# Performance work log

Measured on AMD Instinct MI355X. Metric: run time of the kernel, lower is better.

The kernel has to match this reference:

```python
import jax, jax.numpy as jnp
import numpy as np

B = 4
P0, P1, P2 = 196608, 49152, 12288
DEG = 8
K = 4
EPS = 1e-5


def _cheb_conv(x, cols, vals, W, b):
    """Chebyshev graph conv. x: (B,P,Cin); cols/vals: (P,DEG) fixed-degree sparse L;
    W: (K*Cin, Cout); b: (Cout,). Recursion: T0=x, T1=Lx, Tk=2 L T_{k-1} - T_{k-2}."""
    def lmul(y):  # sparse matvec per batch/channel: (B,P,C) -> (B,P,C)
        return jnp.einsum('pd,bpdc->bpc', vals, y[:, cols, :])
    t0 = x
    t1 = lmul(t0)
    terms = [t0, t1]
    for _ in range(K - 2):
        t2 = 2.0 * lmul(t1) - t0
        terms.append(t2)
        t0, t1 = t1, t2
    xk = jnp.concatenate(terms, axis=-1)  # (B,P,K*Cin)
    return xk @ W + b


def _layernorm(h, g, bt):
    mu = jnp.mean(h, axis=-1, keepdims=True)
    var = jnp.mean(jnp.square(h - mu), axis=-1, keepdims=True)
    return g * (h - mu) / jnp.sqrt(var + EPS) + bt


def _avg_pool4(h):  # HEALPix nested-order average pooling: (B,P,C) -> (B,P//4,C)
    Bh, P, C = h.shape
    return h.reshape(Bh, P // 4, 4, C).mean(axis=2)


def setup_inputs() -> dict:
    key = jax.random.key(0)
    ks = jax.random.split(key, 16)
    cin, c1, c2, c3 = 16, 64, 128, 256
    hid, emb = 512, 256

    def glorot(k, shape):
        fan_in = shape[0]
        return jax.random.normal(k, shape, jnp.float32) / np.sqrt(fan_in)

    inp = {
        'x': jax.random.normal(ks[0], (B, P0, cin), jnp.float32),
        'cols1': jax.random.randint(ks[1], (P0, DEG), 0, P0),
        'vals1': 0.2 * jax.random.normal(ks[2], (P0, DEG), jnp.float32),
        'cols2': jax.random.randint(ks[3], (P1, DEG), 0, P1),
        'vals2': 0.2 * jax.random.normal(ks[4], (P1, DEG), jnp.float32),
        'cols3': jax.random.randint(ks[5], (P2, DEG), 0, P2),
        'vals3': 0.2 * jax.random.normal(ks[6], (P2, DEG), jnp.float32),
        'W1': glorot(ks[7], (K * cin, c1)), 'b1': jnp.zeros((c1,), jnp.float32),
        'g1': jnp.ones((c1,), jnp.float32), 'bt1': jnp.zeros((c1,), jnp.float32),
        'W2': glorot(ks[8], (K * c1, c2)), 'b2': jnp.zeros((c2,), jnp.float32),
        'g2': jnp.ones((c2,), jnp.float32), 'bt2': jnp.zeros((c2,), jnp.float32),
        'W3': glorot(ks[9], (K * c2, c3)), 'b3': jnp.zeros((c3,), jnp.float32),
        'g3': jnp.ones((c3,), jnp.float32), 'bt3': jnp.zeros((c3,), jnp.float32),
        'mW1': glorot(ks[10], (c3, hid)), 'mb1': jnp.zeros((hid,), jnp.float32),
        'mW2': glorot(ks[11], (hid, emb)), 'mb2': jnp.zeros((emb,), jnp.float32),
    }
    return inp


def reference(x, cols1, vals1, cols2, vals2, cols3, vals3,
              W1, b1, g1, bt1, W2, b2, g2, bt2, W3, b3, g3, bt3,
              mW1, mb1, mW2, mb2):
    # Stage 1: ChebConv -> LayerNorm -> ReLU -> avg pool (4:1)
    h = _cheb_conv(x, cols1, vals1, W1, b1)
    h = jax.nn.relu(_layernorm(h, g1, bt1))
    h = _avg_pool4(h)
    # Stage 2
    h = _cheb_conv(h, cols2, vals2, W2, b2)
    h = jax.nn.relu(_layernorm(h, g2, bt2))
    h = _avg_pool4(h)
    # Stage 3 (last stage: no pooling)
    h = _cheb_conv(h, cols3, vals3, W3, b3)
    h = jax.nn.relu(_layernorm(h, g3, bt3))
    # Global mean pool over pixels, then MLP head (Linear-ReLU-Linear)
    z = h.mean(axis=1)                     # (B, 256)
    z = jax.nn.relu(z @ mW1 + mb1)
    z = z @ mW2 + mb2                      # (B, 256)
    return z
```

## Files before the change

### kernel.cpp

```cpp
#include <hip/hip_runtime.h>
#include <hip/hip_bf16.h>

namespace {

constexpr int B  = 4;
constexpr int P0 = 196608, P1 = 49152, P2 = 12288;
constexpr int DEG = 8;
constexpr float EPS = 1e-5f;
constexpr int NBLK3 = (P2 * B) / 64;
constexpr int RSL = 16;
constexpr int RPB = NBLK3 / RSL;

typedef __attribute__((ext_vector_type(4))) float f32x4;
typedef __attribute__((ext_vector_type(8))) short s16x8;

__device__ __forceinline__ float b2f(unsigned short u) {
    union { unsigned int i; float f; } c; c.i = (unsigned int)u << 16; return c.f;
}
__device__ __forceinline__ unsigned short f2b(float f) {
    __hip_bfloat16 h = __float2bfloat16(f);
    return *reinterpret_cast<unsigned short*>(&h);
}

__global__ __launch_bounds__(256)
void x2p_kernel(const float* __restrict__ in, unsigned short* __restrict__ out)
{
    long idx = (long)blockIdx.x * blockDim.x + threadIdx.x;
    if (idx >= (long)P0 * B * 2) return;
    int  h = (int)(idx & 1);
    int  b = (int)((idx >> 1) & 3);
    long p = idx >> 3;
    const float* src = in + ((size_t)b * P0 + p) * 16 + h * 8;
    float4 v0 = *(const float4*)src;
    float4 v1 = *(const float4*)(src + 4);
    union { uint4 u; unsigned short s[8]; } o;
    o.s[0] = f2b(v0.x); o.s[1] = f2b(v0.y); o.s[2] = f2b(v0.z); o.s[3] = f2b(v0.w);
    o.s[4] = f2b(v1.x); o.s[5] = f2b(v1.y); o.s[6] = f2b(v1.z); o.s[7] = f2b(v1.w);
    *(uint4*)&out[((size_t)p * B + b) * 16 + h * 8] = o.u;
}

__global__ __launch_bounds__(256)
void wt_all_kernel(const float* __restrict__ W1, const float* __restrict__ W2,
                   const float* __restrict__ W3,
                   unsigned short* __restrict__ Wt1, unsigned short* __restrict__ Wt2,
                   unsigned short* __restrict__ Wt3)
{
    int i = blockIdx.x * 256 + threadIdx.x;
    if (i < 4096) {
        int n = i % 64, k = i / 64;
        Wt1[n * 64 + k] = f2b(W1[i]);
    } else if (i < 4096 + 32768) {
        int j = i - 4096;
        int n = j % 128, k = j / 128;
        Wt2[n * 256 + k] = f2b(W2[j]);
    } else if (i < 4096 + 32768 + 131072) {
        int j = i - 36864;
        int n = j % 256, k = j / 256;
        Wt3[n * 512 + k] = f2b(W3[j]);
    }
}

template <int CV8>
__global__ __launch_bounds__(256)
void lmul_v2_kernel(const unsigned short* __restrict__ in,
                    const unsigned short* __restrict__ prev,
                    const int* __restrict__ cols, const float* __restrict__ vals,
                    unsigned short* __restrict__ out,
                    float alpha, float beta)
{
    constexpr int ROWS = 256 / CV8;
    __shared__ int   cs[ROWS * DEG];
    __shared__ float vs[ROWS * DEG];
    const int tid = threadIdx.x;
    const long r0 = (long)blockIdx.x * ROWS;
    if (tid < ROWS * DEG) {
        cs[tid] = cols[r0 * DEG + tid];
        vs[tid] = vals[r0 * DEG + tid];
    }
    __syncthreads();

    const int v  = tid & (CV8 - 1);
    const int lr = tid / CV8;
    const uint4* in16 = (const uint4*)in;

    float acc[8] = {0.f,0.f,0.f,0.f,0.f,0.f,0.f,0.f};
#pragma unroll
    for (int d = 0; d < DEG; ++d) {
        int   col = cs[lr * DEG + d];
        float w   = vs[lr * DEG + d];
        union { uint4 u; unsigned short s[8]; } x;
        x.u = in16[(size_t)col * CV8 + v];
#pragma unroll
        for (int j = 0; j < 8; ++j) acc[j] = fmaf(w, b2f(x.s[j]), acc[j]);
    }
    size_t o = (size_t)(r0 + lr) * CV8 + v;
    if (beta != 0.f) {
        union { uint4 u; unsigned short s[8]; } pv;
        pv.u = ((const uint4*)prev)[o];
#pragma unroll
        for (int j = 0; j < 8; ++j)
            acc[j] = fmaf(alpha, acc[j], beta * b2f(pv.s[j]));
    } else if (alpha != 1.f) {
#pragma unroll
        for (int j = 0; j < 8; ++j) acc[j] *= alpha;
    }
    union { uint4 u; unsigned short s[8]; } ou;
#pragma unroll
    for (int j = 0; j < 8; ++j) ou.s[j] = f2b(acc[j]);
    ((uint4*)out)[o] = ou.u;
}

__global__ __launch_bounds__(256)
void s1_mm_kernel(const unsigned short* __restrict__ t0,
                  const unsigned short* __restrict__ t1,
                  const unsigned short* __restrict__ t2,
                  const unsigned short* __restrict__ t3,
                  const unsigned short* __restrict__ Wt,
                  const float* __restrict__ bias,
                  const float* __restrict__ gam,
                  const float* __restrict__ bet,
                  unsigned short* __restrict__ out)
{
    const int wave = threadIdx.x >> 6;
    const int lane = threadIdx.x & 63;
    const int g    = lane >> 4;
    const int c16  = lane & 15;

    s16x8 wf[2][4];
#pragma unroll
    for (int ks = 0; ks < 2; ++ks)
#pragma unroll
        for (int n = 0; n < 4; ++n)
            wf[ks][n] = *(const s16x8*)&Wt[(size_t)(n * 16 + c16) * 64 + ks * 32 + g * 8];

    float bz[4], gz[4], tz[4];
#pragma unroll
    for (int n = 0; n < 4; ++n) {
        bz[n] = bias[n * 16 + c16];
        gz[n] = gam [n * 16 + c16];
        tz[n] = bet [n * 16 + c16];
    }

    const unsigned short* tb[4] = { t0, t1, t2, t3 };
    const int term0  = g >> 1;
    const int coloff = (g & 1) * 8;
    const int bb     = c16 >> 2;
    const int px     = c16 & 3;

    constexpr int NT = P0 / 4;
    const int wg     = blockIdx.x * 4 + wave;
    const int wstep  = gridDim.x * 4;

    for (int t = wg; t < NT; t += wstep) {
        size_t rowbase = ((size_t)(t * 4 + px) * 4 + bb) * 16 + coloff;
        s16x8 a0 = *(const s16x8*)&tb[term0    ][rowbase];
        s16x8 a1 = *(const s16x8*)&tb[term0 + 2][rowbase];

        f32x4 acc[4];
#pragma unroll
        for (int n = 0; n < 4; ++n) acc[n] = (f32x4){bz[n], bz[n], bz[n], bz[n]};
#pragma unroll
        for (int n = 0; n < 4; ++n)
            acc[n] = __builtin_amdgcn_mfma_f32_16x16x32_bf16(a0, wf[0][n], acc[n], 0, 0, 0);
#pragma unroll
        for (int n = 0; n < 4; ++n)
            acc[n] = __builtin_amdgcn_mfma_f32_16x16x32_bf16(a1, wf[1][n], acc[n], 0, 0, 0);

        float s[4] = {0,0,0,0}, q[4] = {0,0,0,0};
#pragma unroll
        for (int n = 0; n < 4; ++n)
#pragma unroll
            for (int r = 0; r < 4; ++r) {
                float v = acc[n][r];
                s[r] += v; q[r] += v * v;
            }
#pragma unroll
        for (int msk = 1; msk < 16; msk <<= 1)
#pragma unroll
            for (int r = 0; r < 4; ++r) {
                s[r] += __shfl_xor(s[r], msk, 64);
                q[r] += __shfl_xor(q[r], msk, 64);
            }
        float mu[4], rs[4];
#pragma unroll
        for (int r = 0; r < 4; ++r) {
            mu[r] = s[r] * (1.f / 64.f);
            float var = q[r] * (1.f / 64.f) - mu[r] * mu[r];
            rs[r] = rsqrtf(var + EPS);
        }
        size_t ro = ((size_t)t * 4 + g) * 64;
#pragma unroll
        for (int n = 0; n < 4; ++n) {
            float pv = 0.f;
#pragma unroll
            for (int r = 0; r < 4; ++r) {
                float h = fmaf(gz[n] * rs[r], acc[n][r] - mu[r], tz[n]);
                pv += fmaxf(h, 0.f);
            }
            out[ro + n * 16 + c16] = f2b(pv * 0.25f);
        }
    }
}

template <int CIN, int COUT, int GM, int GN, int POOL, int LOG2CIN>
__global__ __launch_bounds__(512)
void cheb_mm_v3_kernel(const unsigned short* __restrict__ t0,
                       const unsigned short* __restrict__ t1,
                       const unsigned short* __restrict__ t2,
                       const unsigned short* __restrict__ t3,
                       const unsigned short* __restrict__ Wt,
                       const float* __restrict__ bias,
                       const float* __restrict__ gam,
                       const float* __restrict__ bet,
                       void* __restrict__ outv)
{
    constexpr int KC   = 4 * CIN;
    constexpr int BM   = GM * 64;
    constexpr int NKCH = KC / 64;

    __shared__ unsigned short As[BM * 64];
    __shared__ unsigned short Ws[COUT * 64];
    __shared__ float sq[BM][GN][2];

    const int tid  = threadIdx.x;
    const int wv   = tid >> 6;
    const int gm   = wv / GN;
    const int gn   = wv % GN;
    const int lane = tid & 63;
    const int g    = lane >> 4;
    const int c16  = lane & 15;

    const unsigned short* tb[4] = { t0, t1, t2, t3 };

    float bz[4], gz[4], tz[4];
#pragma unroll
    for (int n = 0; n < 4; ++n) {
        int col = gn * 64 + n * 16 + c16;
        bz[n] = bias[col]; gz[n] = gam[col]; tz[n] = bet[col];
    }

    f32x4 acc[4][4];
#pragma unroll
    for (int m = 0; m < 4; ++m)
#pragma unroll
        for (int n = 0; n < 4; ++n)
            acc[m][n] = (f32x4){bz[n], bz[n], bz[n], bz[n]};

    for (int kc = 0; kc < NKCH; ++kc) {
        if (kc) __syncthreads();
#pragma unroll
        for (int it = 0; it < BM * 8 / 512; ++it) {
            int i = tid + it * 512;
            int row = i >> 3, v = i & 7;
            int k = kc * 64 + v * 8;
            int term = k >> LOG2CIN;
            int c = k & (CIN - 1);
            size_t srow;
            if constexpr (POOL == 4) {
                int pix = blockIdx.x * (BM / 4) + ((row >> 4) << 2) + (row & 3);
                int rb  = (row >> 2) & 3;
                srow = ((size_t)pix * B + rb) * CIN + c;
            } else {
                srow = ((size_t)(blockIdx.x * BM + row)) * CIN + c;
            }
            *(uint4*)((char*)As + row * 128 + ((v * 16) ^ ((row & 7) << 4))) =
                *(const uint4*)&tb[term][srow];
        }
#pragma unroll
        for (int it = 0; it < COUT * 8 / 512; ++it) {
            int i = tid + it * 512;
            int co = i >> 3, v = i & 7;
            *(uint4*)((char*)Ws + co * 128 + ((v * 16) ^ ((co & 7) << 4))) =
                *(const uint4*)&Wt[(size_t)co * KC + kc * 64 + v * 8];
        }
        __syncthreads();
#pragma unroll
        for (int ks = 0; ks < 2; ++ks) {
            const int cb  = ks * 64 + g * 16;
            const int swz = cb ^ ((c16 & 7) << 4);
            s16x8 a[4], bw[4];
#pragma unroll
            for (int m = 0; m < 4; ++m)
                a[m] = *(const s16x8*)((const char*)As + (gm * 64 + m * 16 + c16) * 128 + swz);
#pragma unroll
            for (int n = 0; n < 4; ++n)
                bw[n] = *(const s16x8*)((const char*)Ws + (gn * 64 + n * 16 + c16) * 128 + swz);
#pragma unroll
            for (int n = 0; n < 4; ++n)
#pragma unroll
                for (int m = 0; m < 4; ++m)
                    acc[m][n] = __builtin_amdgcn_mfma_f32_16x16x32_bf16(a[m], bw[n], acc[m][n], 0, 0, 0);
        }
    }

    float sm[4][4], qm[4][4];
#pragma unroll
    for (int m = 0; m < 4; ++m)
#pragma unroll
        for (int r = 0; r < 4; ++r) { sm[m][r] = 0.f; qm[m][r] = 0.f; }
#pragma unroll
    for (int m = 0; m < 4; ++m)
#pragma unroll
        for (int n = 0; n < 4; ++n)
#pragma unroll
            for (int r = 0; r < 4; ++r) {
                float v = acc[m][n][r];
                sm[m][r] += v; qm[m][r] += v * v;
            }
#pragma unroll
    for (int msk = 1; msk < 16; msk <<= 1)
#pragma unroll
        for (int m = 0; m < 4; ++m)
#pragma unroll
            for (int r = 0; r < 4; ++r) {
                sm[m][r] += __shfl_xor(sm[m][r], msk, 64);
                qm[m][r] += __shfl_xor(qm[m][r], msk, 64);
            }
    __syncthreads();
    if (c16 == 0) {
#pragma unroll
        for (int m = 0; m < 4; ++m)
#pragma unroll
            for (int r = 0; r < 4; ++r) {
                sq[gm * 64 + m * 16 + g * 4 + r][gn][0] = sm[m][r];
                sq[gm * 64 + m * 16 + g * 4 + r][gn][1] = qm[m][r];
            }
    }
    __syncthreads();
    float mu[4][4], rs[4][4];
#pragma unroll
    for (int m = 0; m < 4; ++m)
#pragma unroll
        for (int r = 0; r < 4; ++r) {
            int row = gm * 64 + m * 16 + g * 4 + r;
            float ss = 0.f, qq = 0.f;
#pragma unroll
            for (int j = 0; j < GN; ++j) { ss += sq[row][j][0]; qq += sq[row][j][1]; }
            mu[m][r] = ss * (1.f / COUT);
            float var = qq * (1.f / COUT) - mu[m][r] * mu[m][r];
            rs[m][r] = rsqrtf(var + EPS);
        }

    if constexpr (POOL == 4) {
        unsigned short* outp = (unsigned short*)outv;
#pragma unroll
        for (int m = 0; m < 4; ++m) {
            size_t ro = ((size_t)(blockIdx.x * (BM / 16) + gm * 4 + m) * B + g) * COUT + gn * 64;
#pragma unroll
            for (int n = 0; n < 4; ++n) {
                float pv = 0.f;
#pragma unroll
                for (int r = 0; r < 4; ++r) {
                    float h = fmaf(gz[n] * rs[m][r], acc[m][n][r] - mu[m][r], tz[n]);
                    pv += fmaxf(h, 0.f);
                }
                outp[ro + n * 16 + c16] = f2b(pv * 0.25f);
            }
        }
    } else {
        float part[4][4];
#pragma unroll
        for (int n = 0; n < 4; ++n)
#pragma unroll
            for (int r = 0; r < 4; ++r) part[n][r] = 0.f;
#pragma unroll
        for (int m = 0; m < 4; ++m)
#pragma unroll
            for (int n = 0; n < 4; ++n)
#pragma unroll
                for (int r = 0; r < 4; ++r) {
                    float h = fmaf(gz[n] * rs[m][r], acc[m][n][r] - mu[m][r], tz[n]);
                    part[n][r] += fmaxf(h, 0.f);
                }
#pragma unroll
        for (int n = 0; n < 4; ++n)
#pragma unroll
            for (int r = 0; r < 4; ++r) {
                part[n][r] += __shfl_xor(part[n][r], 16, 64);
                part[n][r] += __shfl_xor(part[n][r], 32, 64);
            }
        if (g == 0) {
            float* zb = (float*)outv + ((size_t)(blockIdx.x * GM + gm)) * (B * COUT);
#pragma unroll
            for (int n = 0; n < 4; ++n)
#pragma unroll
                for (int r = 0; r < 4; ++r)
                    zb[(size_t)r * COUT + gn * 64 + n * 16 + c16] = part[n][r];
        }
    }
}

__global__ __launch_bounds__(256)
void zred_kernel(const float* __restrict__ zblk, float* __restrict__ zp2)
{
    int s   = blockIdx.x >> 2;
    int col = (blockIdx.x & 3) * 256 + threadIdx.x;
    float acc = 0.f;
#pragma unroll 8
    for (int r = 0; r < RPB; ++r)
        acc += zblk[(size_t)(s * RPB + r) * (B * 256) + col];
    zp2[(size_t)s * (B * 256) + col] = acc;
}

__global__ __launch_bounds__(512)
void head_kernel(const float* __restrict__ zp2,
                 const float* __restrict__ mW1, const float* __restrict__ mb1,
                 const float* __restrict__ mW2, const float* __restrict__ mb2,
                 float* __restrict__ out)
{
    __shared__ float zs[256];
    __shared__ float hsh[512];
    int b = blockIdx.x, tid = threadIdx.x;
    if (tid < 256) {
        float s = 0.f;
#pragma unroll
        for (int sl = 0; sl < RSL; ++sl)
            s += zp2[(size_t)sl * (B * 256) + b * 256 + tid];
        zs[tid] = s * (1.0f / P2);
    }
    __syncthreads();
    {
        float a = mb1[tid];
#pragma unroll 8
        for (int i = 0; i < 256; ++i) a = fmaf(zs[i], mW1[i * 512 + tid], a);
        hsh[tid] = fmaxf(a, 0.f);
    }
    __syncthreads();
    if (tid < 256) {
        float a = mb2[tid];
#pragma unroll 8
        for (int i = 0; i < 512; ++i) a = fmaf(hsh[i], mW2[i * 256 + tid], a);
        out[(size_t)b * 256 + tid] = a;
    }
}

}

extern "C" void kernel_launch(void* const* d_in, const int* in_sizes, int n_in,
                              void* d_out, int out_size, void* d_ws, size_t ws_size,
                              hipStream_t stream)
{
    const float* x     = (const float*)d_in[0];
    const int*   cols1 = (const int*)  d_in[1];
    const float* vals1 = (const float*)d_in[2];
    const int*   cols2 = (const int*)  d_in[3];
    const float* vals2 = (const float*)d_in[4];
    const int*   cols3 = (const int*)  d_in[5];
    const float* vals3 = (const float*)d_in[6];
    const float* W1  = (const float*)d_in[7];
    const float* b1  = (const float*)d_in[8];
    const float* g1  = (const float*)d_in[9];
    const float* bt1 = (const float*)d_in[10];
    const float* W2  = (const float*)d_in[11];
    const float* b2  = (const float*)d_in[12];
    const float* g2  = (const float*)d_in[13];
    const float* bt2 = (const float*)d_in[14];
    const float* W3  = (const float*)d_in[15];
    const float* b3  = (const float*)d_in[16];
    const float* g3  = (const float*)d_in[17];
    const float* bt3 = (const float*)d_in[18];
    const float* mW1 = (const float*)d_in[19];
    const float* mb1 = (const float*)d_in[20];
    const float* mW2 = (const float*)d_in[21];
    const float* mb2 = (const float*)d_in[22];
    float* out = (float*)d_out;

    char* w = (char*)d_ws;
    size_t off = 0;
    auto alloc = [&](size_t bytes) -> void* {
        void* p = w + off;
        off += (bytes + 255) & ~(size_t)255;
        return p;
    };
    const size_t E1 = (size_t)B * P0 * 16;
    unsigned short* xb  = (unsigned short*)alloc(E1 * 2);
    unsigned short* t_a = (unsigned short*)alloc(E1 * 2);
    unsigned short* t_b = (unsigned short*)alloc(E1 * 2);
    unsigned short* t_c = (unsigned short*)alloc(E1 * 2);
    unsigned short* h1  = (unsigned short*)alloc((size_t)P1 * B * 64 * 2);
    unsigned short* h2  = (unsigned short*)alloc((size_t)P2 * B * 128 * 2);
    unsigned short* Wt1 = (unsigned short*)alloc(64 * 64 * 2);
    unsigned short* Wt2 = (unsigned short*)alloc(256 * 128 * 2);
    unsigned short* Wt3 = (unsigned short*)alloc(512 * 256 * 2);
    float*          zblk = (float*)alloc((size_t)NBLK3 * B * 256 * 4);
    float*          zp2  = (float*)alloc((size_t)RSL * B * 256 * 4);

    x2p_kernel<<<(int)(((long)P0 * B * 2 + 255) / 256), 256, 0, stream>>>(x, xb);
    wt_all_kernel<<<(4096 + 32768 + 131072 + 255) / 256, 256, 0, stream>>>(
        W1, W2, W3, Wt1, Wt2, Wt3);

    {
        lmul_v2_kernel<8><<<P0 / 32, 256, 0, stream>>>(xb,  nullptr, cols1, vals1, t_a, 1.f,  0.f);
        lmul_v2_kernel<8><<<P0 / 32, 256, 0, stream>>>(t_a, xb,      cols1, vals1, t_b, 2.f, -1.f);
        lmul_v2_kernel<8><<<P0 / 32, 256, 0, stream>>>(t_b, t_a,     cols1, vals1, t_c, 2.f, -1.f);
        s1_mm_kernel<<<2048, 256, 0, stream>>>(xb, t_a, t_b, t_c, Wt1, b1, g1, bt1, h1);
    }
    {
        lmul_v2_kernel<32><<<P1 / 8, 256, 0, stream>>>(h1,  nullptr, cols2, vals2, t_a, 1.f,  0.f);
        lmul_v2_kernel<32><<<P1 / 8, 256, 0, stream>>>(t_a, h1,      cols2, vals2, t_b, 2.f, -1.f);
        lmul_v2_kernel<32><<<P1 / 8, 256, 0, stream>>>(t_b, t_a,     cols2, vals2, t_c, 2.f, -1.f);
        cheb_mm_v3_kernel<64, 128, 4, 2, 4, 6><<<(P1 * B) / 256, 512, 0, stream>>>(
            h1, t_a, t_b, t_c, Wt2, b2, g2, bt2, h2);
    }
    {
        lmul_v2_kernel<64><<<P2 / 4, 256, 0, stream>>>(h2,  nullptr, cols3, vals3, t_a, 1.f,  0.f);
        lmul_v2_kernel<64><<<P2 / 4, 256, 0, stream>>>(t_a, h2,      cols3, vals3, t_b, 2.f, -1.f);
        lmul_v2_kernel<64><<<P2 / 4, 256, 0, stream>>>(t_b, t_a,     cols3, vals3, t_c, 2.f, -1.f);
        cheb_mm_v3_kernel<128, 256, 2, 4, 1, 7><<<(P2 * B) / 128, 512, 0, stream>>>(
            h2, t_a, t_b, t_c, Wt3, b3, g3, bt3, zblk);
    }
    zred_kernel<<<RSL * 4, 256, 0, stream>>>(zblk, zp2);
    head_kernel<<<B, 512, 0, stream>>>(zp2, mW1, mb1, mW2, mb2, out);

    (void)in_sizes; (void)n_in; (void)out_size; (void)ws_size;
}
```

Baseline: 420.9 us.

## Split MLP head into two parallel kernels with transposed weights

Replaces the single 4-block head kernel with two kernels, headA (16 blocks) and headB (8 blocks). Each computes output columns for all four batches, reading weights as contiguous float4 rows and splitting the reduction across two thread groups. The head weights are transposed inside the existing weight-prep kernel so each output column reads a contiguous row. The goal is more parallelism and better memory access in the tail of the pipeline, which was serialized on 4 blocks. It costs an extra kernel launch plus extra transpose work over about 260K more elements in the prep kernel.

```diff
diff --git a/kernel.cpp b/kernel.cpp
--- a/kernel.cpp
+++ b/kernel.cpp
@@ -42,21 +42,31 @@
 __global__ __launch_bounds__(256)
 void wt_all_kernel(const float* __restrict__ W1, const float* __restrict__ W2,
                    const float* __restrict__ W3,
+                   const float* __restrict__ mW1, const float* __restrict__ mW2,
                    unsigned short* __restrict__ Wt1, unsigned short* __restrict__ Wt2,
-                   unsigned short* __restrict__ Wt3)
+                   unsigned short* __restrict__ Wt3,
+                   float* __restrict__ mW1t, float* __restrict__ mW2t)
 {
     int i = blockIdx.x * 256 + threadIdx.x;
     if (i < 4096) {
         int n = i % 64, k = i / 64;
         Wt1[n * 64 + k] = f2b(W1[i]);
-    } else if (i < 4096 + 32768) {
+    } else if (i < 36864) {
         int j = i - 4096;
         int n = j % 128, k = j / 128;
         Wt2[n * 256 + k] = f2b(W2[j]);
-    } else if (i < 4096 + 32768 + 131072) {
+    } else if (i < 167936) {
         int j = i - 36864;
         int n = j % 256, k = j / 256;
         Wt3[n * 512 + k] = f2b(W3[j]);
+    } else if (i < 299008) {
+        int j = i - 167936;
+        int n = j % 512, k = j / 512;
+        mW1t[(size_t)n * 256 + k] = mW1[j];
+    } else if (i < 430080) {
+        int j = i - 299008;
+        int n = j % 256, k = j / 256;
+        mW2t[(size_t)n * 512 + k] = mW2[j];
     }
 }
 
@@ -402,36 +412,61 @@
     zp2[(size_t)s * (B * 256) + col] = acc;
 }
 
-__global__ __launch_bounds__(512)
-void head_kernel(const float* __restrict__ zp2,
-                 const float* __restrict__ mW1, const float* __restrict__ mb1,
-                 const float* __restrict__ mW2, const float* __restrict__ mb2,
-                 float* __restrict__ out)
-{
-    __shared__ float zs[256];
-    __shared__ float hsh[512];
-    int b = blockIdx.x, tid = threadIdx.x;
-    if (tid < 256) {
+__global__ __launch_bounds__(256)
+void headA_kernel(const float* __restrict__ zp2, const float* __restrict__ mW1t,
+                  const float* __restrict__ mb1, float* __restrict__ hh)
+{
+    __shared__ float zs[B * 256];
+    __shared__ float ph[256];
+    const int tid = threadIdx.x;
+    for (int idx = tid; idx < B * 256; idx += 256) {
         float s = 0.f;
 #pragma unroll
-        for (int sl = 0; sl < RSL; ++sl)
-            s += zp2[(size_t)sl * (B * 256) + b * 256 + tid];
-        zs[tid] = s * (1.0f / P2);
-    }
-    __syncthreads();
-    {
-        float a = mb1[tid];
-#pragma unroll 8
-        for (int i = 0; i < 256; ++i) a = fmaf(zs[i], mW1[i * 512 + tid], a);
-        hsh[tid] = fmaxf(a, 0.f);
-    }
-    __syncthreads();
-    if (tid < 256) {
-        float a = mb2[tid];
-#pragma unroll 8
-        for (int i = 0; i < 512; ++i) a = fmaf(hsh[i], mW2[i * 256 + tid], a);
-        out[(size_t)b * 256 + tid] = a;
-    }
+        for (int sl = 0; sl < RSL; ++sl) s += zp2[(size_t)sl * (B * 256) + idx];
+        zs[idx] = s * (1.f / P2);
+    }
+    __syncthreads();
+    const int jl = tid & 31, b = (tid >> 5) & 3, ig = tid >> 7;
+    const int j  = blockIdx.x * 32 + jl;
+    const float4* wrow = (const float4*)&mW1t[(size_t)j * 256 + ig * 128];
+    const float*  zb   = &zs[b * 256 + ig * 128];
+    float acc = 0.f;
+#pragma unroll
+    for (int i4 = 0; i4 < 32; ++i4) {
+        float4 wv = wrow[i4];
+        acc += zb[i4*4]*wv.x + zb[i4*4+1]*wv.y + zb[i4*4+2]*wv.z + zb[i4*4+3]*wv.w;
+    }
+    ph[tid] = acc;
+    __syncthreads();
+    if (tid < 128) {
+        float a = ph[tid] + ph[tid + 128] + mb1[j];
+        hh[b * 512 + j] = fmaxf(a, 0.f);
+    }
+}
+
+__global__ __launch_bounds__(256)
+void headB_kernel(const float* __restrict__ hh, const float* __restrict__ mW2t,
+                  const float* __restrict__ mb2, float* __restrict__ out)
+{
+    __shared__ float hs[B * 512];
+    __shared__ float ph[256];
+    const int tid = threadIdx.x;
+    for (int idx = tid; idx < B * 512; idx += 256) hs[idx] = hh[idx];
+    __syncthreads();
+    const int cl = tid & 31, b = (tid >> 5) & 3, ig = tid >> 7;
+    const int c  = blockIdx.x * 32 + cl;
+    const float4* wrow = (const float4*)&mW2t[(size_t)c * 512 + ig * 256];
+    const float*  hb   = &hs[b * 512 + ig * 256];
+    float acc = 0.f;
+#pragma unroll
+    for (int j4 = 0; j4 < 64; ++j4) {
+        float4 wv = wrow[j4];
+        acc += hb[j4*4]*wv.x + hb[j4*4+1]*wv.y + hb[j4*4+2]*wv.z + hb[j4*4+3]*wv.w;
+    }
+    ph[tid] = acc;
+    __syncthreads();
+    if (tid < 128)
+        out[b * 256 + c] = ph[tid] + ph[tid + 128] + mb2[c];
 }
 
 }
@@ -482,12 +517,15 @@
     unsigned short* Wt1 = (unsigned short*)alloc(64 * 64 * 2);
     unsigned short* Wt2 = (unsigned short*)alloc(256 * 128 * 2);
     unsigned short* Wt3 = (unsigned short*)alloc(512 * 256 * 2);
+    float*          mW1t = (float*)alloc((size_t)512 * 256 * 4);
+    float*          mW2t = (float*)alloc((size_t)256 * 512 * 4);
     float*          zblk = (float*)alloc((size_t)NBLK3 * B * 256 * 4);
     float*          zp2  = (float*)alloc((size_t)RSL * B * 256 * 4);
+    float*          hh   = (float*)alloc((size_t)B * 512 * 4);
 
     x2p_kernel<<<(int)(((long)P0 * B * 2 + 255) / 256), 256, 0, stream>>>(x, xb);
-    wt_all_kernel<<<(4096 + 32768 + 131072 + 255) / 256, 256, 0, stream>>>(
-        W1, W2, W3, Wt1, Wt2, Wt3);
+    wt_all_kernel<<<(430080 + 255) / 256, 256, 0, stream>>>(
+        W1, W2, W3, mW1, mW2, Wt1, Wt2, Wt3, mW1t, mW2t);
 
     {
         lmul_v2_kernel<8><<<P0 / 32, 256, 0, stream>>>(xb,  nullptr, cols1, vals1, t_a, 1.f,  0.f);
@@ -510,7 +548,8 @@
             h2, t_a, t_b, t_c, Wt3, b3, g3, bt3, zblk);
     }
     zred_kernel<<<RSL * 4, 256, 0, stream>>>(zblk, zp2);
-    head_kernel<<<B, 512, 0, stream>>>(zp2, mW1, mb1, mW2, mb2, out);
+    headA_kernel<<<16, 256, 0, stream>>>(zp2, mW1t, mb1, hh);
+    headB_kernel<<<8, 256, 0, stream>>>(hh, mW2t, mb2, out);
 
     (void)in_sizes; (void)n_in; (void)out_size; (void)ws_size;
 }
```

After: 407.2 us. -3.3%, faster.
